# Optimization experiments

Hardware: AMD Instinct MI355X
Metric: run time of the kernel (lower is better)

The kernel has to match this reference:

```python
import jax, jax.numpy as jnp
import numpy as np

N = 500_000
D = 256
D_OUT = 256
B = 16_384


def setup_inputs() -> dict:
    key = jax.random.key(0)
    ks = jax.random.split(key, 10)
    x = jax.random.normal(ks[0], (N, D), dtype=jnp.float32)
    batch = jnp.sort(jax.random.randint(ks[1], (N,), 0, B))
    last_click_mask = jax.random.uniform(ks[2], (N,), dtype=jnp.float32)
    s = 1.0 / np.sqrt(D)
    W1 = jax.random.uniform(ks[3], (D, D), jnp.float32, -s, s)
    b1 = jax.random.uniform(ks[4], (D,), jnp.float32, -s, s)
    W2 = jax.random.uniform(ks[5], (D, D), jnp.float32, -s, s)
    b2 = jax.random.uniform(ks[6], (D,), jnp.float32, -s, s)
    w3 = jax.random.uniform(ks[7], (D, 1), jnp.float32, -s, s)
    s4 = 1.0 / np.sqrt(2 * D)
    W4 = jax.random.uniform(ks[8], (2 * D, D_OUT), jnp.float32, -s4, s4)
    b4 = jax.random.uniform(ks[9], (D_OUT,), jnp.float32, -s4, s4)
    return {
        "x": x,
        "batch": batch,
        "last_click_mask": last_click_mask,
        "num_segments": B,
        "W1": W1, "b1": b1, "W2": W2, "b2": b2,
        "w3": w3, "W4": W4, "b4": b4,
    }


def reference(x, batch, last_click_mask, num_segments, W1, b1, W2, b2, w3, W4, b4):
    # local_rep = global_add_pool(x * mask, batch)  -> [B, D]
    local_rep = jax.ops.segment_sum(x * last_click_mask[:, None], batch,
                                    num_segments=num_segments)
    local_rep_repeat = local_rep[batch]                       # [N, D] gather
    att = jax.nn.sigmoid(local_rep_repeat @ W1 + b1 + x @ W2 + b2) @ w3  # [N, 1]
    weighted_x = x * att                                      # [N, D]
    global_rep = jax.ops.segment_sum(weighted_x, batch,
                                     num_segments=num_segments)  # [B, D]
    rep = jnp.concatenate([local_rep, global_rep], axis=1)    # [B, 2D]
    return rep @ W4 + b4                                      # [B, D_OUT]
```

## Files before the change

kernel.cpp:

```cpp
#include <hip/hip_runtime.h>
#include <hip/hip_bf16.h>

#define NROWS 500000
#define DIM   256
#define BSEG  16384
#define LDSP  264
#define NTILE 7813
#define TILE_B (64 * LDSP * 2)

typedef __attribute__((ext_vector_type(8))) short short8;
typedef __attribute__((ext_vector_type(4))) float floatx4;

#define GLD16(gsrc, ldst)                                                      \
  __builtin_amdgcn_global_load_lds(                                            \
      (const __attribute__((address_space(1))) unsigned int*)(gsrc),           \
      (__attribute__((address_space(3))) unsigned int*)(ldst), 16, 0, 0)


__device__ __forceinline__ unsigned short f2bf(float f) {
  unsigned u = __float_as_uint(f);
  unsigned r = u + 0x7fffu + ((u >> 16) & 1u);
  return (unsigned short)(r >> 16);
}
__device__ __forceinline__ float bf2f(short s) {
  return __uint_as_float(((unsigned)(unsigned short)s) << 16);
}
__device__ __forceinline__ int imin(int a, int b) { return a < b ? a : b; }

__global__ __launch_bounds__(256) void k_init(
    const float* __restrict__ W1, const float* __restrict__ W2,
    const float* __restrict__ W4, short* __restrict__ W1t,
    short* __restrict__ W2t, short* __restrict__ W4t,
    float* __restrict__ zbase)
{
  int blk = blockIdx.x;
  int n = threadIdx.x;
  if (blk < 32) {
    const float* W; short* out; int kt;
    if (blk < 8)       { W = W1; out = W1t; kt = blk; }
    else if (blk < 16) { W = W2; out = W2t; kt = blk - 8; }
    else               { W = W4; out = W4t; kt = blk - 16; }
    short tmp[32];
#pragma unroll
    for (int kk = 0; kk < 32; ++kk)
      tmp[kk] = (short)f2bf(W[(size_t)(kt * 32 + kk) * DIM + n]);
    size_t base = ((size_t)kt * 256 + n) * 32;
#pragma unroll
    for (int kk = 0; kk < 32; kk += 4)
      *(short4*)&out[base + kk] = *(short4*)&tmp[kk];
  } else {
    int i = (blk - 32) * 256 + n;
    ((float4*)zbase)[i] = make_float4(0.f, 0.f, 0.f, 0.f);
  }
}

__device__ __forceinline__ void stage_tile(const float* __restrict__ A, int row0,
                                           int maxrow, short* xs, int tid)
{
#pragma unroll
  for (int it = 0; it < 16; ++it) {
    int linear = it * 256 + tid;
    int r = linear >> 6;
    int c4 = linear & 63;
    int row = imin(row0 + r, maxrow);
    float4 v = *(const float4*)&A[(size_t)row * DIM + c4 * 4];
    short4 o;
    o.x = (short)f2bf(v.x); o.y = (short)f2bf(v.y);
    o.z = (short)f2bf(v.z); o.w = (short)f2bf(v.w);
    *(short4*)&xs[r * LDSP + c4 * 4] = o;
  }
}

__global__ __launch_bounds__(256) void k_prep(
    const float* __restrict__ x, const int* __restrict__ batch,
    const float* __restrict__ mask, char* __restrict__ xbf16p,
    float* __restrict__ local_rep)
{
  __shared__ __align__(16) short xs[64 * LDSP];
  __shared__ int   seg_s[64];
  __shared__ float mask_s[64];
  const int tid = threadIdx.x;
  const int tile = (int)blockIdx.x;
  const int row0 = tile * 64;

  stage_tile(x, row0, NROWS - 1, xs, tid);
  if (tid < 64) {
    int row = imin(row0 + tid, NROWS - 1);
    seg_s[tid] = batch[row];
    mask_s[tid] = mask[row];
  }
  __syncthreads();

  float4* g4 = (float4*)(xbf16p + (size_t)tile * TILE_B);
  const float4* l4 = (const float4*)xs;
#pragma unroll
  for (int j = 0; j < 8; ++j)
    g4[j * 256 + tid] = l4[j * 256 + tid];
  if (tid < 64) g4[2048 + tid] = l4[2048 + tid];

  const int col = tid;
  const int rmax = imin(64, NROWS - row0);
  float acc = 0.f;
  int cur = seg_s[0];
  for (int r = 0; r < rmax; ++r) {
    int s = seg_s[r];
    float xv = bf2f(xs[r * LDSP + col]);
    if (s != cur) {
      atomicAdd(&local_rep[(size_t)cur * DIM + col], acc);
      acc = 0.f; cur = s;
    }
    acc = fmaf(xv, mask_s[r], acc);
  }
  atomicAdd(&local_rep[(size_t)cur * DIM + col], acc);
}

__device__ __forceinline__ void mfma_pass(const short* xs, const short* __restrict__ Wt,
                                          floatx4 acc[4][4], int lane15, int quad, int n0)
{
  for (int kt = 0; kt < 8; ++kt) {
    short8 bfr[4], afr[4];
#pragma unroll
    for (int jn = 0; jn < 4; ++jn)
      bfr[jn] = *(const short8*)&Wt[(size_t)kt * 8192 + (n0 + jn * 16 + lane15) * 32 + quad * 8];
#pragma unroll
    for (int i = 0; i < 4; ++i)
      afr[i] = *(const short8*)&xs[(i * 16 + lane15) * LDSP + kt * 32 + quad * 8];
#pragma unroll
    for (int i = 0; i < 4; ++i)
#pragma unroll
      for (int jn = 0; jn < 4; ++jn)
        acc[i][jn] = __builtin_amdgcn_mfma_f32_16x16x32_bf16(afr[i], bfr[jn], acc[i][jn], 0, 0, 0);
  }
}

__global__ __launch_bounds__(256) void k_h1_mfma(
    const float* __restrict__ A, const short* __restrict__ Wt,
    const float* __restrict__ bias, short* __restrict__ H1bf)
{
  __shared__ __align__(16) short xs[64 * LDSP];
  const int tid = threadIdx.x;
  const int row0 = (int)blockIdx.x * 64;
  stage_tile(A, row0, BSEG - 1, xs, tid);
  __syncthreads();
  const int lane = tid & 63, wave = tid >> 6;
  const int lane15 = lane & 15, quad = lane >> 4;
  const int n0 = wave * 64;
  floatx4 acc[4][4];
#pragma unroll
  for (int i = 0; i < 4; ++i)
#pragma unroll
    for (int j = 0; j < 4; ++j) acc[i][j] = (floatx4)0.f;
  mfma_pass(xs, Wt, acc, lane15, quad, n0);
#pragma unroll
  for (int i = 0; i < 4; ++i)
#pragma unroll
    for (int jn = 0; jn < 4; ++jn) {
      int col = n0 + jn * 16 + lane15;
      float bv = bias[col];
#pragma unroll
      for (int r = 0; r < 4; ++r) {
        int row = row0 + i * 16 + quad * 4 + r;
        H1bf[(size_t)row * DIM + col] = (short)f2bf(acc[i][jn][r] + bv);
      }
    }
}

__global__ __launch_bounds__(256) void k_fused_main(
    const char* __restrict__ xbf16p, const int* __restrict__ batch,
    const short* __restrict__ W2t, const float* __restrict__ b2,
    const float* __restrict__ w3, const short* __restrict__ H1bf,
    float* __restrict__ global_rep)
{
  __shared__ __align__(16) short xs[64 * LDSP];
  __shared__ int   seg_s[64];
  __shared__ float att_s[64];
  const int tid = threadIdx.x;
  const int bid = (int)blockIdx.x;
  const int row0 = bid * 64;
  const int lane = tid & 63, wave = tid >> 6;

  {
    const char* gtile = xbf16p + (size_t)bid * TILE_B;
    char* lbase = (char*)xs;
#pragma unroll
    for (int j = 0; j < 9; ++j) {
      int c = wave + 4 * j;
      if (c < 33)
        GLD16(gtile + (size_t)c * 1024 + lane * 16, lbase + c * 1024);
    }
  }
  if (tid < 64) {
    seg_s[tid] = batch[imin(row0 + tid, NROWS - 1)];
    att_s[tid] = 0.f;
  }
  __syncthreads();

  const int lane15 = lane & 15, quad = lane >> 4;
  const int n0 = wave * 64;
  floatx4 acc[4][4];
#pragma unroll
  for (int i = 0; i < 4; ++i)
#pragma unroll
    for (int j = 0; j < 4; ++j) acc[i][j] = (floatx4)0.f;
  mfma_pass(xs, W2t, acc, lane15, quad, n0);

  float b2v[4], w3v[4];
#pragma unroll
  for (int jn = 0; jn < 4; ++jn) {
    int col = n0 + jn * 16 + lane15;
    b2v[jn] = b2[col];
    w3v[jn] = w3[col];
  }
  float part[4][4];
  int prev_seg = -1;
  float h[4] = {0.f, 0.f, 0.f, 0.f};
#pragma unroll
  for (int i = 0; i < 4; ++i)
#pragma unroll
    for (int r = 0; r < 4; ++r) {
      int rl = i * 16 + quad * 4 + r;
      int seg = seg_s[rl];
      if (seg != prev_seg) {
#pragma unroll
        for (int jn = 0; jn < 4; ++jn)
          h[jn] = bf2f(H1bf[(size_t)seg * DIM + n0 + jn * 16 + lane15]);
        prev_seg = seg;
      }
      float p = 0.f;
#pragma unroll
      for (int jn = 0; jn < 4; ++jn) {
        float z = acc[i][jn][r] + h[jn] + b2v[jn];
        float sg = __builtin_amdgcn_rcpf(1.0f + __expf(-z));
        p = fmaf(sg, w3v[jn], p);
      }
      part[i][r] = p;
    }
#pragma unroll
  for (int off = 1; off < 16; off <<= 1)
#pragma unroll
    for (int i = 0; i < 4; ++i)
#pragma unroll
      for (int r = 0; r < 4; ++r)
        part[i][r] += __shfl_xor(part[i][r], off, 64);
  if (lane15 == 0) {
#pragma unroll
    for (int i = 0; i < 4; ++i)
#pragma unroll
      for (int r = 0; r < 4; ++r)
        atomicAdd(&att_s[i * 16 + quad * 4 + r], part[i][r]);
  }
  __syncthreads();

  const int col = tid;
  const int rmax = imin(64, NROWS - row0);
  float acc2 = 0.f;
  int cur = seg_s[0];
  for (int r = 0; r < rmax; ++r) {
    int s = seg_s[r];
    float xv = bf2f(xs[r * LDSP + col]);
    float av = att_s[r];
    if (s != cur) {
      atomicAdd(&global_rep[(size_t)cur * DIM + col], acc2);
      acc2 = 0.f; cur = s;
    }
    acc2 = fmaf(xv, av, acc2);
  }
  atomicAdd(&global_rep[(size_t)cur * DIM + col], acc2);
}

__global__ __launch_bounds__(256) void k_out_mfma(
    const float* __restrict__ local_rep, const float* __restrict__ global_rep,
    const short* __restrict__ W4t, const float* __restrict__ b4,
    float* __restrict__ out)
{
  __shared__ __align__(16) short xs[64 * LDSP];
  const int tid = threadIdx.x;
  const int row0 = (int)blockIdx.x * 64;
  const int lane = tid & 63, wave = tid >> 6;
  const int lane15 = lane & 15, quad = lane >> 4;
  const int n0 = wave * 64;
  floatx4 acc[4][4];
#pragma unroll
  for (int i = 0; i < 4; ++i)
#pragma unroll
    for (int j = 0; j < 4; ++j) acc[i][j] = (floatx4)0.f;

  stage_tile(local_rep, row0, BSEG - 1, xs, tid);
  __syncthreads();
  mfma_pass(xs, W4t, acc, lane15, quad, n0);
  __syncthreads();
  stage_tile(global_rep, row0, BSEG - 1, xs, tid);
  __syncthreads();
  mfma_pass(xs, W4t + (size_t)8 * 8192, acc, lane15, quad, n0);

#pragma unroll
  for (int i = 0; i < 4; ++i)
#pragma unroll
    for (int jn = 0; jn < 4; ++jn) {
      int col = n0 + jn * 16 + lane15;
      float bv = b4[col];
#pragma unroll
      for (int r = 0; r < 4; ++r) {
        int row = row0 + i * 16 + quad * 4 + r;
        out[(size_t)row * DIM + col] = acc[i][jn][r] + bv;
      }
    }
}

extern "C" void kernel_launch(void* const* d_in, const int* in_sizes, int n_in,
                              void* d_out, int out_size, void* d_ws, size_t ws_size,
                              hipStream_t stream) {
  (void)in_sizes; (void)n_in; (void)out_size; (void)ws_size;
  const float* x    = (const float*)d_in[0];
  const int*   batch= (const int*)d_in[1];
  const float* mask = (const float*)d_in[2];
  const float* W1 = (const float*)d_in[4];
  const float* b1 = (const float*)d_in[5];
  const float* W2 = (const float*)d_in[6];
  const float* b2 = (const float*)d_in[7];
  const float* w3 = (const float*)d_in[8];
  const float* W4 = (const float*)d_in[9];
  const float* b4 = (const float*)d_in[10];
  float* out = (float*)d_out;

  char* base = (char*)d_ws;
  float* local_rep  = (float*)(base);
  float* global_rep = (float*)(base + (size_t)16 * 1024 * 1024);
  short* H1bf       = (short*)(base + (size_t)32 * 1024 * 1024);
  short* W1t        = (short*)(base + (size_t)40 * 1024 * 1024);
  short* W2t        = (short*)(base + (size_t)40 * 1024 * 1024 + 128 * 1024);
  short* W4t        = (short*)(base + (size_t)40 * 1024 * 1024 + 256 * 1024);
  char*  xbf16p     = base + (size_t)48 * 1024 * 1024;

  hipLaunchKernelGGL(k_init, dim3(32 + 8192), dim3(256), 0, stream,
                     W1, W2, W4, W1t, W2t, W4t, local_rep);

  hipLaunchKernelGGL(k_prep, dim3(NTILE), dim3(256), 0, stream,
                     x, batch, mask, xbf16p, local_rep);

  hipLaunchKernelGGL(k_h1_mfma, dim3(BSEG / 64), dim3(256), 0, stream,
                     local_rep, W1t, b1, H1bf);

  hipLaunchKernelGGL(k_fused_main, dim3(NTILE), dim3(256), 0, stream,
                     xbf16p, batch, W2t, b2, w3, H1bf, global_rep);

  hipLaunchKernelGGL(k_out_mfma, dim3(BSEG / 64), dim3(256), 0, stream,
                     local_rep, global_rep, W4t, b4, out);
}
```

Baseline: 979.9 us.

## Halve row tiles to 32 in prep and fused main kernels for occupancy

Replaces the 64-row prep and fused attention/pooling kernels with 32-row versions that use half the LDS and registers, with launch-bound hints to fit more blocks per CU. The prep kernel writes the bf16 image directly to global memory alongside LDS instead of copying it out after a barrier. The fused kernel prefetches H1 and bias values before the MFMA pass. Smaller tiles double the block count and raise the number of segment-boundary atomics per row, and they reuse each W2 fragment across fewer rows.

```diff
diff --git a/kernel.cpp b/kernel.cpp
--- a/kernel.cpp
+++ b/kernel.cpp
@@ -5,8 +5,8 @@
 #define DIM   256
 #define BSEG  16384
 #define LDSP  264
-#define NTILE 7813
-#define TILE_B (64 * LDSP * 2)
+#define NT32  15625
+#define TILE32_B 17408
 
 typedef __attribute__((ext_vector_type(8))) short short8;
 typedef __attribute__((ext_vector_type(4))) float floatx4;
@@ -52,6 +52,52 @@
     int i = (blk - 32) * 256 + n;
     ((float4*)zbase)[i] = make_float4(0.f, 0.f, 0.f, 0.f);
   }
+}
+
+__global__ __launch_bounds__(256, 6) void k_prep32(
+    const float* __restrict__ x, const int* __restrict__ batch,
+    const float* __restrict__ mask, char* __restrict__ xbf16p,
+    float* __restrict__ local_rep)
+{
+  __shared__ __align__(16) short xs[32 * LDSP];
+  __shared__ int   seg_s[32];
+  __shared__ float mask_s[32];
+  const int tid = threadIdx.x;
+  const int tile = (int)blockIdx.x;
+  const int row0 = tile * 32;
+
+  if (tid < 32) {
+    seg_s[tid]  = batch[row0 + tid];
+    mask_s[tid] = mask[row0 + tid];
+  }
+  short* img = (short*)(xbf16p + (size_t)tile * TILE32_B);
+#pragma unroll
+  for (int it = 0; it < 8; ++it) {
+    int linear = it * 256 + tid;
+    int r  = linear >> 6;
+    int c4 = linear & 63;
+    float4 v = *(const float4*)&x[(size_t)(row0 + r) * DIM + c4 * 4];
+    short4 o;
+    o.x = (short)f2bf(v.x); o.y = (short)f2bf(v.y);
+    o.z = (short)f2bf(v.z); o.w = (short)f2bf(v.w);
+    *(short4*)&xs[r * LDSP + c4 * 4] = o;
+    *(short4*)&img[r * LDSP + c4 * 4] = o;
+  }
+  __syncthreads();
+
+  const int col = tid;
+  float acc = 0.f;
+  int cur = seg_s[0];
+  for (int r = 0; r < 32; ++r) {
+    int s = seg_s[r];
+    float xv = bf2f(xs[r * LDSP + col]);
+    if (s != cur) {
+      atomicAdd(&local_rep[(size_t)cur * DIM + col], acc);
+      acc = 0.f; cur = s;
+    }
+    acc = fmaf(xv, mask_s[r], acc);
+  }
+  atomicAdd(&local_rep[(size_t)cur * DIM + col], acc);
 }
 
 __device__ __forceinline__ void stage_tile(const float* __restrict__ A, int row0,
@@ -71,49 +117,6 @@
   }
 }
 
-__global__ __launch_bounds__(256) void k_prep(
-    const float* __restrict__ x, const int* __restrict__ batch,
-    const float* __restrict__ mask, char* __restrict__ xbf16p,
-    float* __restrict__ local_rep)
-{
-  __shared__ __align__(16) short xs[64 * LDSP];
-  __shared__ int   seg_s[64];
-  __shared__ float mask_s[64];
-  const int tid = threadIdx.x;
-  const int tile = (int)blockIdx.x;
-  const int row0 = tile * 64;
-
-  stage_tile(x, row0, NROWS - 1, xs, tid);
-  if (tid < 64) {
-    int row = imin(row0 + tid, NROWS - 1);
-    seg_s[tid] = batch[row];
-    mask_s[tid] = mask[row];
-  }
-  __syncthreads();
-
-  float4* g4 = (float4*)(xbf16p + (size_t)tile * TILE_B);
-  const float4* l4 = (const float4*)xs;
-#pragma unroll
-  for (int j = 0; j < 8; ++j)
-    g4[j * 256 + tid] = l4[j * 256 + tid];
-  if (tid < 64) g4[2048 + tid] = l4[2048 + tid];
-
-  const int col = tid;
-  const int rmax = imin(64, NROWS - row0);
-  float acc = 0.f;
-  int cur = seg_s[0];
-  for (int r = 0; r < rmax; ++r) {
-    int s = seg_s[r];
-    float xv = bf2f(xs[r * LDSP + col]);
-    if (s != cur) {
-      atomicAdd(&local_rep[(size_t)cur * DIM + col], acc);
-      acc = 0.f; cur = s;
-    }
-    acc = fmaf(xv, mask_s[r], acc);
-  }
-  atomicAdd(&local_rep[(size_t)cur * DIM + col], acc);
-}
-
 __device__ __forceinline__ void mfma_pass(const short* xs, const short* __restrict__ Wt,
                                           floatx4 acc[4][4], int lane15, int quad, int n0)
 {
@@ -127,6 +130,25 @@
       afr[i] = *(const short8*)&xs[(i * 16 + lane15) * LDSP + kt * 32 + quad * 8];
 #pragma unroll
     for (int i = 0; i < 4; ++i)
+#pragma unroll
+      for (int jn = 0; jn < 4; ++jn)
+        acc[i][jn] = __builtin_amdgcn_mfma_f32_16x16x32_bf16(afr[i], bfr[jn], acc[i][jn], 0, 0, 0);
+  }
+}
+
+__device__ __forceinline__ void mfma_pass32(const short* xs, const short* __restrict__ Wt,
+                                            floatx4 acc[2][4], int lane15, int quad, int n0)
+{
+  for (int kt = 0; kt < 8; ++kt) {
+    short8 bfr[4], afr[2];
+#pragma unroll
+    for (int jn = 0; jn < 4; ++jn)
+      bfr[jn] = *(const short8*)&Wt[(size_t)kt * 8192 + (n0 + jn * 16 + lane15) * 32 + quad * 8];
+#pragma unroll
+    for (int i = 0; i < 2; ++i)
+      afr[i] = *(const short8*)&xs[(i * 16 + lane15) * LDSP + kt * 32 + quad * 8];
+#pragma unroll
+    for (int i = 0; i < 2; ++i)
 #pragma unroll
       for (int jn = 0; jn < 4; ++jn)
         acc[i][jn] = __builtin_amdgcn_mfma_f32_16x16x32_bf16(afr[i], bfr[jn], acc[i][jn], 0, 0, 0);
@@ -165,45 +187,36 @@
     }
 }
 
-__global__ __launch_bounds__(256) void k_fused_main(
+__global__ __launch_bounds__(256, 5) void k_fused32(
     const char* __restrict__ xbf16p, const int* __restrict__ batch,
     const short* __restrict__ W2t, const float* __restrict__ b2,
     const float* __restrict__ w3, const short* __restrict__ H1bf,
     float* __restrict__ global_rep)
 {
-  __shared__ __align__(16) short xs[64 * LDSP];
-  __shared__ int   seg_s[64];
-  __shared__ float att_s[64];
+  __shared__ __align__(16) short xs[TILE32_B / 2];
+  __shared__ int   seg_s[32];
+  __shared__ float att_s[32];
   const int tid = threadIdx.x;
   const int bid = (int)blockIdx.x;
-  const int row0 = bid * 64;
+  const int row0 = bid * 32;
   const int lane = tid & 63, wave = tid >> 6;
-
-  {
-    const char* gtile = xbf16p + (size_t)bid * TILE_B;
-    char* lbase = (char*)xs;
-#pragma unroll
-    for (int j = 0; j < 9; ++j) {
-      int c = wave + 4 * j;
-      if (c < 33)
-        GLD16(gtile + (size_t)c * 1024 + lane * 16, lbase + c * 1024);
-    }
-  }
-  if (tid < 64) {
-    seg_s[tid] = batch[imin(row0 + tid, NROWS - 1)];
-    att_s[tid] = 0.f;
-  }
-  __syncthreads();
-
   const int lane15 = lane & 15, quad = lane >> 4;
   const int n0 = wave * 64;
-  floatx4 acc[4][4];
-#pragma unroll
-  for (int i = 0; i < 4; ++i)
-#pragma unroll
-    for (int j = 0; j < 4; ++j) acc[i][j] = (floatx4)0.f;
-  mfma_pass(xs, W2t, acc, lane15, quad, n0);
-
+
+  {
+    const char* gtile = xbf16p + (size_t)bid * TILE32_B;
+    char* lbase = (char*)xs;
+#pragma unroll
+    for (int j = 0; j < 5; ++j) {
+      int c = wave + 4 * j;
+      if (c < 17)
+        GLD16(gtile + (size_t)c * 1024 + lane * 16, lbase + c * 1024);
+    }
+  }
+  if (tid < 32) {
+    seg_s[tid] = batch[row0 + tid];
+    att_s[tid] = 0.f;
+  }
   float b2v[4], w3v[4];
 #pragma unroll
   for (int jn = 0; jn < 4; ++jn) {
@@ -211,11 +224,24 @@
     b2v[jn] = b2[col];
     w3v[jn] = w3[col];
   }
-  float part[4][4];
-  int prev_seg = -1;
-  float h[4] = {0.f, 0.f, 0.f, 0.f};
-#pragma unroll
-  for (int i = 0; i < 4; ++i)
+  __syncthreads();
+
+  int prev_seg = seg_s[quad * 4];
+  float h[4];
+#pragma unroll
+  for (int jn = 0; jn < 4; ++jn)
+    h[jn] = bf2f(H1bf[(size_t)prev_seg * DIM + n0 + jn * 16 + lane15]);
+
+  floatx4 acc[2][4];
+#pragma unroll
+  for (int i = 0; i < 2; ++i)
+#pragma unroll
+    for (int j = 0; j < 4; ++j) acc[i][j] = (floatx4)0.f;
+  mfma_pass32(xs, W2t, acc, lane15, quad, n0);
+
+  float part[2][4];
+#pragma unroll
+  for (int i = 0; i < 2; ++i)
 #pragma unroll
     for (int r = 0; r < 4; ++r) {
       int rl = i * 16 + quad * 4 + r;
@@ -238,13 +264,13 @@
 #pragma unroll
   for (int off = 1; off < 16; off <<= 1)
 #pragma unroll
-    for (int i = 0; i < 4; ++i)
+    for (int i = 0; i < 2; ++i)
 #pragma unroll
       for (int r = 0; r < 4; ++r)
         part[i][r] += __shfl_xor(part[i][r], off, 64);
   if (lane15 == 0) {
 #pragma unroll
-    for (int i = 0; i < 4; ++i)
+    for (int i = 0; i < 2; ++i)
 #pragma unroll
       for (int r = 0; r < 4; ++r)
         atomicAdd(&att_s[i * 16 + quad * 4 + r], part[i][r]);
@@ -252,10 +278,9 @@
   __syncthreads();
 
   const int col = tid;
-  const int rmax = imin(64, NROWS - row0);
   float acc2 = 0.f;
   int cur = seg_s[0];
-  for (int r = 0; r < rmax; ++r) {
+  for (int r = 0; r < 32; ++r) {
     int s = seg_s[r];
     float xv = bf2f(xs[r * LDSP + col]);
     float av = att_s[r];
@@ -335,13 +360,13 @@
   hipLaunchKernelGGL(k_init, dim3(32 + 8192), dim3(256), 0, stream,
                      W1, W2, W4, W1t, W2t, W4t, local_rep);
 
-  hipLaunchKernelGGL(k_prep, dim3(NTILE), dim3(256), 0, stream,
+  hipLaunchKernelGGL(k_prep32, dim3(NT32), dim3(256), 0, stream,
                      x, batch, mask, xbf16p, local_rep);
 
   hipLaunchKernelGGL(k_h1_mfma, dim3(BSEG / 64), dim3(256), 0, stream,
                      local_rep, W1t, b1, H1bf);
 
-  hipLaunchKernelGGL(k_fused_main, dim3(NTILE), dim3(256), 0, stream,
+  hipLaunchKernelGGL(k_fused32, dim3(NT32), dim3(256), 0, stream,
                      xbf16p, batch, W2t, b2, w3, H1bf, global_rep);
 
   hipLaunchKernelGGL(k_out_mfma, dim3(BSEG / 64), dim3(256), 0, stream,
```

Result: faster. 960.4 us (-2.0%).
